# Performance work log

Hardware: AMD Instinct MI355X
Metric: run time of the kernel (lower is better)

The kernel has to match this reference:

```python
import jax, jax.numpy as jnp
import numpy as np

DIM = 512
HEADS = 8
HEAD_DIM = DIM // HEADS
WINDOW = 128
TOKEN_SELF_ATTN_VALUE = -5e4  # lucidrains local-attention constant for shared_qk self mask


def setup_inputs() -> dict:
    key = jax.random.key(0)
    k1, k2, k3, k4 = jax.random.split(key, 4)
    B, N = 4, 8192
    x = jax.random.normal(k1, (B, N, DIM), dtype=jnp.float32)
    w_qkv = jax.random.normal(k2, (3 * DIM, DIM), dtype=jnp.float32) * (DIM ** -0.5)
    w_proj = jax.random.normal(k3, (DIM, DIM), dtype=jnp.float32) * (DIM ** -0.5)
    b_proj = jax.random.normal(k4, (DIM,), dtype=jnp.float32) * 0.01
    return {"x": x, "w_qkv": w_qkv, "w_proj": w_proj, "b_proj": b_proj}


def _look_around(b):
    # b: [B,H,nw,w,D] -> [B,H,nw,2w,D] = concat(prev_window, cur_window); window 0 padded with zeros
    padded = jnp.pad(b, ((0, 0), (0, 0), (1, 0), (0, 0), (0, 0)))
    return jnp.concatenate([padded[:, :, :-1], b], axis=3)


def _local_attn(q, k, v):
    # causal sliding-window attention, window=128, look_backward=1, shared_qk
    B, H, N, D = q.shape
    w = WINDOW
    nw = N // w
    scale = D ** -0.5
    # shared_qk: l2-normalize keys (F.normalize, eps=1e-12)
    k = k / jnp.clip(jnp.linalg.norm(k, axis=-1, keepdims=True), 1e-12, None)

    bq = q.reshape(B, H, nw, w, D)
    bk = _look_around(k.reshape(B, H, nw, w, D))  # [B,H,nw,2w,D]
    bv = _look_around(v.reshape(B, H, nw, w, D))

    t = jnp.arange(N).reshape(nw, w)
    t_pad = jnp.pad(t, ((1, 0), (0, 0)), constant_values=-1)
    bq_t = t                                         # [nw, w]
    bq_k = jnp.concatenate([t_pad[:-1], t], axis=1)  # [nw, 2w]

    sim = jnp.einsum('bhwie,bhwje->bhwij', bq, bk) * scale  # [B,H,nw,w,2w]

    self_mask = bq_t[:, :, None] == bq_k[:, None, :]
    causal_mask = bq_t[:, :, None] < bq_k[:, None, :]
    pad_mask = (bq_k == -1)[:, None, :]
    mask_value = -jnp.finfo(sim.dtype).max
    sim = jnp.where(self_mask, TOKEN_SELF_ATTN_VALUE, sim)
    sim = jnp.where(causal_mask | pad_mask, mask_value, sim)

    attn = jax.nn.softmax(sim, axis=-1)  # dropout is identity in eval mode
    out = jnp.einsum('bhwij,bhwje->bhwie', attn, bv)
    return out.reshape(B, H, N, D)


def reference(x, w_qkv, w_proj, b_proj):
    B, N, C = x.shape
    qkv = x @ w_qkv.T  # [B,N,3C]
    q, k, v = jnp.split(qkv, 3, axis=-1)
    to_heads = lambda t: t.reshape(B, N, HEADS, HEAD_DIM).transpose(0, 2, 1, 3)
    out = _local_attn(to_heads(q), to_heads(k), to_heads(v))  # [B,H,N,D]
    out = out.transpose(0, 2, 1, 3).reshape(B, N, C)
    return out @ w_proj.T + b_proj
```

## Files before the change

### kernel.cpp

```cpp
#include <hip/hip_runtime.h>
#include <stdint.h>

typedef uint16_t u16;
typedef __bf16 bf16x8 __attribute__((ext_vector_type(8)));
typedef float f32x4 __attribute__((ext_vector_type(4)));
typedef uint16_t u16x4 __attribute__((ext_vector_type(4)));
typedef uint16_t u16x8 __attribute__((ext_vector_type(8)));

typedef __attribute__((address_space(1))) void as1_void;
typedef __attribute__((address_space(3))) void as3_void;

__device__ __forceinline__ float bf2f(u16 b) {
    union { uint32_t u; float f; } v; v.u = ((uint32_t)b) << 16; return v.f;
}
__device__ __forceinline__ u16 f2bf(float f) {
    union { float f; uint32_t u; } v; v.f = f;
    uint32_t u = v.u;
    u += 0x7fffu + ((u >> 16) & 1u);
    return (u16)(u >> 16);
}
__device__ __forceinline__ void gload_lds16(const u16* g, u16* l) {
    __builtin_amdgcn_global_load_lds((as1_void*)g, (as3_void*)l, 16, 0, 0);
}

__global__ __launch_bounds__(256) void cvt_w(
    const float* __restrict__ wq, u16* __restrict__ wqb,
    const float* __restrict__ wp, u16* __restrict__ wpb)
{
    const float* src; u16* dst; int base;
    const int b = blockIdx.x;
    if (b < 384) { src = wq; dst = wqb; base = b; }
    else         { src = wp; dst = wpb; base = b - 384; }
    const size_t i = ((size_t)base * 256 + threadIdx.x) * 8;
    f32x4 a = *(const f32x4*)(src + i);
    f32x4 c = *(const f32x4*)(src + i + 4);
    u16x8 o;
    o[0] = f2bf(a[0]); o[1] = f2bf(a[1]); o[2] = f2bf(a[2]); o[3] = f2bf(a[3]);
    o[4] = f2bf(c[0]); o[5] = f2bf(c[1]); o[6] = f2bf(c[2]); o[7] = f2bf(c[3]);
    *(u16x8*)(dst + i) = o;
}

template<int NT, bool NORMK>
__global__ __launch_bounds__(256, 3) void gemm_a32(
    const float* __restrict__ A, int lda,
    const u16* __restrict__ B, int ldb,
    u16* __restrict__ C, int ldc)
{
    __shared__ float lA[2][128 * 32];
    __shared__ u16   lB[2][128 * 32];

    const int tid  = threadIdx.x;
    const int lane = tid & 63;
    const int wave = tid >> 6;
    const int wr = (wave >> 1) * 64;
    const int wc = (wave & 1) * 64;
    const int cl = lane & 15;
    const int gr = lane >> 4;

    int fid = blockIdx.y * gridDim.x + blockIdx.x;
    const int nwg = gridDim.x * gridDim.y;
    fid = (fid & 7) * (nwg >> 3) + (fid >> 3);
    const int row0 = (fid / gridDim.x) * 128;
    const int col0 = (fid % gridDim.x) * 128;

    const int srowA = lane >> 3;
    const int schA  = ((lane & 7) - srowA) & 7;
    const int srowB = lane >> 2;
    const int schB  = ((lane & 3) - ((lane >> 3) & 3)) & 3;

    f32x4 acc[4][4] = {};

    auto STAGE = [&](int t, int d) {
        const int k0 = t * 32;
        #pragma unroll
        for (int i = 0; i < 4; ++i) {
            const int Rg = wave * 32 + i * 8;
            gload_lds16((const u16*)(A + (size_t)(row0 + Rg + srowA) * lda + k0 + schA * 4),
                        (u16*)&lA[d][Rg * 32]);
        }
        #pragma unroll
        for (int i = 0; i < 2; ++i) {
            const int Rg = wave * 16 + i * 64;
            gload_lds16(B + (size_t)(col0 + Rg + srowB) * ldb + k0 + schB * 8,
                        &lB[d][Rg * 32]);
        }
    };

    STAGE(0, 0);
    STAGE(1, 1);
    #pragma unroll
    for (int t = 0; t < NT; ++t) {
        if (t < NT - 1) asm volatile("s_waitcnt vmcnt(6)" ::: "memory");
        else            asm volatile("s_waitcnt vmcnt(0)" ::: "memory");
        __builtin_amdgcn_s_barrier();
        const float* la = lA[t & 1];
        const u16*   lb = lB[t & 1];

        bf16x8 af[4], bfv[4];
        #pragma unroll
        for (int m = 0; m < 4; ++m) {
            const int ra = wr + m * 16 + cl;
            const int s0 = (gr * 2 + ra) & 7;
            const int s1 = (gr * 2 + 1 + ra) & 7;
            const f32x4 x0 = *(const f32x4*)&la[ra * 32 + s0 * 4];
            const f32x4 x1 = *(const f32x4*)&la[ra * 32 + s1 * 4];
            bf16x8 t8;
            t8[0] = (__bf16)x0[0]; t8[1] = (__bf16)x0[1];
            t8[2] = (__bf16)x0[2]; t8[3] = (__bf16)x0[3];
            t8[4] = (__bf16)x1[0]; t8[5] = (__bf16)x1[1];
            t8[6] = (__bf16)x1[2]; t8[7] = (__bf16)x1[3];
            af[m] = t8;
        }
        #pragma unroll
        for (int n = 0; n < 4; ++n) {
            const int rb = wc + n * 16 + cl;
            bfv[n] = *(const bf16x8*)&lb[rb * 32 + ((gr + (rb >> 1)) & 3) * 8];
        }
        __builtin_amdgcn_s_setprio(1);
        #pragma unroll
        for (int m = 0; m < 4; ++m)
            #pragma unroll
            for (int n = 0; n < 4; ++n)
                acc[m][n] = __builtin_amdgcn_mfma_f32_16x16x32_bf16(af[m], bfv[n], acc[m][n], 0, 0, 0);
        __builtin_amdgcn_s_setprio(0);
        __builtin_amdgcn_s_barrier();
        if (t + 2 < NT) STAGE(t + 2, t & 1);
    }

    if constexpr (NORMK) {
        if (col0 + wc >= 512 && col0 + wc < 1024) {
            #pragma unroll
            for (int m = 0; m < 4; ++m)
                #pragma unroll
                for (int j = 0; j < 4; ++j) {
                    float ss = 0.f;
                    #pragma unroll
                    for (int n = 0; n < 4; ++n) ss += acc[m][n][j] * acc[m][n][j];
                    ss += __shfl_xor(ss, 1);
                    ss += __shfl_xor(ss, 2);
                    ss += __shfl_xor(ss, 4);
                    ss += __shfl_xor(ss, 8);
                    const float scl = 1.f / fmaxf(sqrtf(ss), 1e-12f);
                    #pragma unroll
                    for (int n = 0; n < 4; ++n) acc[m][n][j] *= scl;
                }
        }
    }

    #pragma unroll
    for (int m = 0; m < 4; ++m) {
        const int r = row0 + wr + m * 16 + gr * 4;
        #pragma unroll
        for (int n = 0; n < 4; ++n) {
            const int c = col0 + wc + n * 16 + cl;
            #pragma unroll
            for (int j = 0; j < 4; ++j)
                C[(size_t)(r + j) * ldc + c] = f2bf(acc[m][n][j]);
        }
    }
}

template<int NT, bool C_F32, bool NORMK>
__global__ __launch_bounds__(512) void gemm256(
    const u16* __restrict__ A, int lda,
    const u16* __restrict__ B, int ldb,
    const float* __restrict__ bias,
    void* __restrict__ Cv, int ldc)
{
    __shared__ u16 lA[2][256 * 64];
    __shared__ u16 lB[2][256 * 64];

    const int tid  = threadIdx.x;
    const int lane = tid & 63;
    const int wave = tid >> 6;
    const int wm = wave >> 2;
    const int wn = wave & 3;
    const int cl = lane & 15;
    const int gr = lane >> 4;

    int fid = blockIdx.y * gridDim.x + blockIdx.x;
    const int nwg = gridDim.x * gridDim.y;
    fid = (fid & 7) * (nwg >> 3) + (fid >> 3);
    const int row0 = (fid / gridDim.x) * 256;
    const int col0 = (fid % gridDim.x) * 256;

    const int srow   = lane >> 3;
    const int schunk = ((lane & 7) - srow) & 7;

    f32x4 acc[8][4] = {};

    auto STAGE = [&](int t, int d) {
        const int k0 = t * 64;
        #pragma unroll
        for (int i = 0; i < 4; ++i) {
            const int Rg = wave * 32 + i * 8;
            gload_lds16(A + (size_t)(row0 + Rg + srow) * lda + k0 + schunk * 8,
                        &lA[d][Rg * 64]);
            gload_lds16(B + (size_t)(col0 + Rg + srow) * ldb + k0 + schunk * 8,
                        &lB[d][Rg * 64]);
        }
    };

    auto COMPUTE = [&](int d) {
        const u16* la = lA[d];
        const u16* lb = lB[d];
        bf16x8 bfrag[2][4];
        #pragma unroll
        for (int kk = 0; kk < 2; ++kk)
            #pragma unroll
            for (int n = 0; n < 4; ++n) {
                const int rb = wn * 64 + n * 16 + cl;
                bfrag[kk][n] = *(const bf16x8*)(lb + rb * 64 + (((kk * 4 + gr + rb) & 7) * 8));
            }
        __builtin_amdgcn_s_setprio(1);
        #pragma unroll
        for (int m = 0; m < 8; ++m) {
            const int ra = wm * 128 + m * 16 + cl;
            const bf16x8 a0 = *(const bf16x8*)(la + ra * 64 + (((gr + ra) & 7) * 8));
            const bf16x8 a1 = *(const bf16x8*)(la + ra * 64 + (((4 + gr + ra) & 7) * 8));
            #pragma unroll
            for (int n = 0; n < 4; ++n)
                acc[m][n] = __builtin_amdgcn_mfma_f32_16x16x32_bf16(a0, bfrag[0][n], acc[m][n], 0, 0, 0);
            #pragma unroll
            for (int n = 0; n < 4; ++n)
                acc[m][n] = __builtin_amdgcn_mfma_f32_16x16x32_bf16(a1, bfrag[1][n], acc[m][n], 0, 0, 0);
        }
        __builtin_amdgcn_s_setprio(0);
    };

    STAGE(0, 0);
    STAGE(1, 1);
    #pragma unroll
    for (int t = 0; t < NT; ++t) {
        if (t < NT - 1) asm volatile("s_waitcnt vmcnt(8)" ::: "memory");
        else            asm volatile("s_waitcnt vmcnt(0)" ::: "memory");
        __builtin_amdgcn_s_barrier();
        COMPUTE(t & 1);
        __builtin_amdgcn_s_barrier();
        if (t + 2 < NT) STAGE(t + 2, t & 1);
    }

    if constexpr (NORMK) {
        if (col0 + wn * 64 >= 512 && col0 + wn * 64 < 1024) {
            #pragma unroll
            for (int m = 0; m < 8; ++m)
                #pragma unroll
                for (int j = 0; j < 4; ++j) {
                    float ss = 0.f;
                    #pragma unroll
                    for (int n = 0; n < 4; ++n) ss += acc[m][n][j] * acc[m][n][j];
                    ss += __shfl_xor(ss, 1);
                    ss += __shfl_xor(ss, 2);
                    ss += __shfl_xor(ss, 4);
                    ss += __shfl_xor(ss, 8);
                    const float scl = 1.f / fmaxf(sqrtf(ss), 1e-12f);
                    #pragma unroll
                    for (int n = 0; n < 4; ++n) acc[m][n][j] *= scl;
                }
        }
    }

    #pragma unroll
    for (int m = 0; m < 8; ++m) {
        const int r = row0 + wm * 128 + m * 16 + gr * 4;
        #pragma unroll
        for (int n = 0; n < 4; ++n) {
            const int c = col0 + wn * 64 + n * 16 + cl;
            const float bv = bias ? bias[c] : 0.f;
            #pragma unroll
            for (int j = 0; j < 4; ++j) {
                const float val = acc[m][n][j] + bv;
                if constexpr (C_F32) ((float*)Cv)[(size_t)(r + j) * ldc + c] = val;
                else                 ((u16*)Cv)[(size_t)(r + j) * ldc + c] = f2bf(val);
            }
        }
    }
}

template<bool A_F32, bool C_F32, bool NORMK>
__global__ __launch_bounds__(256) void gemm_bt_f32(
    const void* __restrict__ Av, int lda,
    const float* __restrict__ B, int ldb,
    const float* __restrict__ bias,
    void* __restrict__ Cv, int ldc,
    int K)
{
    __shared__ u16 lA[128 * 32];
    __shared__ u16 lB[128 * 32];

    const int tid  = threadIdx.x;
    const int lane = tid & 63;
    const int wave = tid >> 6;
    const int wr   = (wave >> 1) * 64;
    const int wc   = (wave & 1) * 64;
    const int row0 = blockIdx.y * 128;
    const int col0 = blockIdx.x * 128;

    f32x4 acc[4][4] = {};

    for (int k0 = 0; k0 < K; k0 += 32) {
        #pragma unroll
        for (int i = 0; i < 4; ++i) {
            const int idx = i * 256 + tid;
            const int r = idx >> 3;
            const int p = (idx & 7) * 4;
            u16x4 a4, b4;
            if constexpr (A_F32) {
                const float* Af = (const float*)Av;
                f32x4 va = *(const f32x4*)(Af + (size_t)(row0 + r) * lda + k0 + p);
                a4[0] = f2bf(va[0]); a4[1] = f2bf(va[1]); a4[2] = f2bf(va[2]); a4[3] = f2bf(va[3]);
            } else {
                const u16* Ab = (const u16*)Av;
                a4 = *(const u16x4*)(Ab + (size_t)(row0 + r) * lda + k0 + p);
            }
            {
                f32x4 vb = *(const f32x4*)(B + (size_t)(col0 + r) * ldb + k0 + p);
                b4[0] = f2bf(vb[0]); b4[1] = f2bf(vb[1]); b4[2] = f2bf(vb[2]); b4[3] = f2bf(vb[3]);
            }
            *(u16x4*)&lA[r * 32 + p] = a4;
            *(u16x4*)&lB[r * 32 + p] = b4;
        }
        __syncthreads();

        bf16x8 af[4], bfv[4];
        #pragma unroll
        for (int m = 0; m < 4; ++m)
            af[m] = *(const bf16x8*)(lA + (wr + m * 16 + (lane & 15)) * 32 + (lane >> 4) * 8);
        #pragma unroll
        for (int n = 0; n < 4; ++n)
            bfv[n] = *(const bf16x8*)(lB + (wc + n * 16 + (lane & 15)) * 32 + (lane >> 4) * 8);
        #pragma unroll
        for (int m = 0; m < 4; ++m)
            #pragma unroll
            for (int n = 0; n < 4; ++n)
                acc[m][n] = __builtin_amdgcn_mfma_f32_16x16x32_bf16(af[m], bfv[n], acc[m][n], 0, 0, 0);
        __syncthreads();
    }

    if constexpr (NORMK) {
        if (col0 >= 512 && col0 < 1024) {
            #pragma unroll
            for (int m = 0; m < 4; ++m)
                #pragma unroll
                for (int j = 0; j < 4; ++j) {
                    float ss = 0.f;
                    #pragma unroll
                    for (int n = 0; n < 4; ++n) ss += acc[m][n][j] * acc[m][n][j];
                    ss += __shfl_xor(ss, 1);
                    ss += __shfl_xor(ss, 2);
                    ss += __shfl_xor(ss, 4);
                    ss += __shfl_xor(ss, 8);
                    const float scl = 1.f / fmaxf(sqrtf(ss), 1e-12f);
                    #pragma unroll
                    for (int n = 0; n < 4; ++n) acc[m][n][j] *= scl;
                }
        }
    }

    #pragma unroll
    for (int m = 0; m < 4; ++m) {
        const int r = row0 + wr + m * 16 + ((lane >> 4) << 2);
        #pragma unroll
        for (int n = 0; n < 4; ++n) {
            const int c = col0 + wc + n * 16 + (lane & 15);
            const float bv = bias ? bias[c] : 0.f;
            #pragma unroll
            for (int j = 0; j < 4; ++j) {
                const float val = acc[m][n][j] + bv;
                if constexpr (C_F32) ((float*)Cv)[(size_t)(r + j) * ldc + c] = val;
                else                 ((u16*)Cv)[(size_t)(r + j) * ldc + c] = f2bf(val);
            }
        }
    }
}

__global__ __launch_bounds__(512, 4) void attn_kernel(const u16* qkv, u16* o)
{
    constexpr int CC = 1536;
    constexpr int NTOK = 8192;
    constexpr int KP = 72;
    constexpr int VP = 136;
    constexpr int PP = 136;
    __shared__ u16 kn[128 * KP];
    __shared__ u16 vT[64 * VP];
    __shared__ u16 Pl[128 * PP];

    const int tid  = threadIdx.x;
    const int lane = tid & 63;
    const int wave = tid >> 6;
    const int cl = lane & 15;
    const int gr = lane >> 4;

    int blk = blockIdx.x;
    blk = (blk & 7) * (gridDim.x >> 3) + (blk >> 3);

    const int iw  = blk & 63;
    const int h   = (blk >> 6) & 7;
    const int b   = blk >> 9;

    const int tq0 = iw * 128;
    const size_t rowbase = (size_t)b * NTOK;
    const u16* qbase = qkv + rowbase * CC + h * 64;
    const u16* kbase = qbase + 512;
    const u16* vbase = qbase + 1024;

    const int wrow = wave * 16;
    bf16x8 qf[2];
    #pragma unroll
    for (int kk = 0; kk < 2; ++kk)
        qf[kk] = *(const bf16x8*)(qbase + (size_t)(tq0 + wrow + cl) * CC + kk * 32 + gr * 8);

    f32x4 oacc[4] = {};
    float m_run[4] = {-3.0e38f, -3.0e38f, -3.0e38f, -3.0e38f};
    float l_run[4] = {0.f, 0.f, 0.f, 0.f};

    for (int c = 0; c < 2; ++c) {
        const int tkc = tq0 - 128 + c * 128;

        #pragma unroll
        for (int p = 0; p < 2; ++p) {
            const int id = tid + p * 512;
            const int row = id >> 3, dc = id & 7;
            u16x8 v8 = {};
            if (tkc >= 0) v8 = *(const u16x8*)(kbase + (size_t)(tkc + row) * CC + dc * 8);
            *(u16x8*)&kn[row * KP + dc * 8] = v8;
        }
        #pragma unroll
        for (int p = 0; p < 2; ++p) {
            const int id = tid + p * 512;
            const int key = id & 127, dc = id >> 7;
            u16x8 v8 = {};
            if (tkc >= 0) v8 = *(const u16x8*)(vbase + (size_t)(tkc + key) * CC + dc * 8);
            #pragma unroll
            for (int e = 0; e < 8; ++e) vT[(dc * 8 + e) * VP + key] = v8[e];
        }
        __syncthreads();

        f32x4 s[8] = {};
        #pragma unroll
        for (int n = 0; n < 8; ++n)
            #pragma unroll
            for (int kk = 0; kk < 2; ++kk) {
                const bf16x8 kf = *(const bf16x8*)&kn[(n * 16 + cl) * KP + kk * 32 + gr * 8];
                s[n] = __builtin_amdgcn_mfma_f32_16x16x32_bf16(qf[kk], kf, s[n], 0, 0, 0);
            }

        float pmax[4] = {-3.0e38f, -3.0e38f, -3.0e38f, -3.0e38f};
        #pragma unroll
        for (int n = 0; n < 8; ++n) {
            const int tkk = tkc + n * 16 + cl;
            const bool pad = tkk < 0;
            #pragma unroll
            for (int j = 0; j < 4; ++j) {
                const int tq = tq0 + wrow + gr * 4 + j;
                float sv = s[n][j] * 0.125f;
                const int rel = tkk - tq;
                sv = (rel == 0) ? -5.0e4f : sv;
                sv = (rel > 0 || pad) ? -6.0e4f : sv;
                s[n][j] = sv;
                pmax[j] = fmaxf(pmax[j], sv);
            }
        }
        float cold[4];
        #pragma unroll
        for (int j = 0; j < 4; ++j) {
            pmax[j] = fmaxf(pmax[j], __shfl_xor(pmax[j], 1));
            pmax[j] = fmaxf(pmax[j], __shfl_xor(pmax[j], 2));
            pmax[j] = fmaxf(pmax[j], __shfl_xor(pmax[j], 4));
            pmax[j] = fmaxf(pmax[j], __shfl_xor(pmax[j], 8));
            const float mn = fmaxf(m_run[j], pmax[j]);
            cold[j] = __expf(m_run[j] - mn);
            m_run[j] = mn;
            l_run[j] *= cold[j];
        }
        #pragma unroll
        for (int n = 0; n < 8; ++n)
            #pragma unroll
            for (int j = 0; j < 4; ++j) {
                const float p = __expf(s[n][j] - m_run[j]);
                s[n][j] = p;
                l_run[j] += p;
            }
        #pragma unroll
        for (int n = 0; n < 4; ++n) {
            f32x4 t = oacc[n];
            t[0] *= cold[0]; t[1] *= cold[1]; t[2] *= cold[2]; t[3] *= cold[3];
            oacc[n] = t;
        }
        #pragma unroll
        for (int n = 0; n < 8; ++n)
            #pragma unroll
            for (int j = 0; j < 4; ++j)
                Pl[(wrow + gr * 4 + j) * PP + n * 16 + cl] = f2bf(s[n][j]);
        __syncthreads();

        #pragma unroll
        for (int kk = 0; kk < 4; ++kk) {
            const bf16x8 pa = *(const bf16x8*)&Pl[(wrow + cl) * PP + kk * 32 + gr * 8];
            #pragma unroll
            for (int n = 0; n < 4; ++n) {
                const bf16x8 vb = *(const bf16x8*)&vT[(n * 16 + cl) * VP + kk * 32 + gr * 8];
                oacc[n] = __builtin_amdgcn_mfma_f32_16x16x32_bf16(pa, vb, oacc[n], 0, 0, 0);
            }
        }
        __syncthreads();
    }

    float inv[4];
    #pragma unroll
    for (int j = 0; j < 4; ++j) {
        l_run[j] += __shfl_xor(l_run[j], 1);
        l_run[j] += __shfl_xor(l_run[j], 2);
        l_run[j] += __shfl_xor(l_run[j], 4);
        l_run[j] += __shfl_xor(l_run[j], 8);
        inv[j] = 1.f / l_run[j];
    }
    u16* obase = o + rowbase * CC + h * 64;
    const int r0 = tq0 + wrow + gr * 4;
    #pragma unroll
    for (int n = 0; n < 4; ++n) {
        const int d = n * 16 + cl;
        #pragma unroll
        for (int j = 0; j < 4; ++j)
            obase[(size_t)(r0 + j) * CC + d] = f2bf(oacc[n][j] * inv[j]);
    }
}

extern "C" void kernel_launch(void* const* d_in, const int* in_sizes, int n_in,
                              void* d_out, int out_size, void* d_ws, size_t ws_size,
                              hipStream_t stream)
{
    (void)in_sizes; (void)n_in; (void)out_size;
    const float* x      = (const float*)d_in[0];
    const float* w_qkv  = (const float*)d_in[1];
    const float* w_proj = (const float*)d_in[2];
    const float* b_proj = (const float*)d_in[3];
    float* out = (float*)d_out;

    const int BN = 4 * 8192;
    const size_t qkv_b = (size_t)BN * 1536 * 2;
    const size_t wq_b  = (size_t)1536 * 512 * 2;
    const size_t wp_b  = (size_t)512 * 512 * 2;

    uint8_t* p = (uint8_t*)d_ws;
    u16* qkv = (u16*)p;

    if (ws_size >= qkv_b + wq_b + wp_b) {
        u16* wqb = (u16*)(p + qkv_b);
        u16* wpb = (u16*)(p + qkv_b + wq_b);
        cvt_w<<<512, 256, 0, stream>>>(w_qkv, wqb, w_proj, wpb);
        gemm_a32<16, true><<<dim3(12, 256), 256, 0, stream>>>(
            x, 512, wqb, 512, qkv, 1536);
        attn_kernel<<<dim3(4 * 8 * 64), 512, 0, stream>>>(qkv, qkv);
        gemm256<8, true, false><<<dim3(2, 128), 512, 0, stream>>>(
            qkv, 1536, wpb, 512, b_proj, out, 512);
    } else {
        gemm_bt_f32<true, false, true><<<dim3(12, BN / 128), 256, 0, stream>>>(
            x, 512, w_qkv, 512, nullptr, qkv, 1536, 512);
        attn_kernel<<<dim3(4 * 8 * 64), 512, 0, stream>>>(qkv, qkv);
        gemm_bt_f32<false, true, false><<<dim3(4, BN / 128), 256, 0, stream>>>(
            qkv, 1536, w_proj, 512, b_proj, out, 512, 512);
    }
}
```

Before: 180.5 us.

## Stage fp32 A tile through registers and store as bf16 in LDS

```diff
diff --git a/kernel.cpp b/kernel.cpp
--- a/kernel.cpp
+++ b/kernel.cpp
@@ -41,13 +41,13 @@
 }
 
 template<int NT, bool NORMK>
-__global__ __launch_bounds__(256, 3) void gemm_a32(
+__global__ __launch_bounds__(256, 4) void gemm_rs(
     const float* __restrict__ A, int lda,
     const u16* __restrict__ B, int ldb,
     u16* __restrict__ C, int ldc)
 {
-    __shared__ float lA[2][128 * 32];
-    __shared__ u16   lB[2][128 * 32];
+    __shared__ u16 lA[2][128 * 32];
+    __shared__ u16 lB[2][128 * 32];
 
     const int tid  = threadIdx.x;
     const int lane = tid & 63;
@@ -63,54 +63,57 @@
     const int row0 = (fid / gridDim.x) * 128;
     const int col0 = (fid % gridDim.x) * 128;
 
-    const int srowA = lane >> 3;
-    const int schA  = ((lane & 7) - srowA) & 7;
+    const int arow = tid >> 1;
+    const int ah   = tid & 1;
     const int srowB = lane >> 2;
     const int schB  = ((lane & 3) - ((lane >> 3) & 3)) & 3;
 
+    f32x4 S[4];
+
     f32x4 acc[4][4] = {};
 
-    auto STAGE = [&](int t, int d) {
-        const int k0 = t * 32;
-        #pragma unroll
-        for (int i = 0; i < 4; ++i) {
-            const int Rg = wave * 32 + i * 8;
-            gload_lds16((const u16*)(A + (size_t)(row0 + Rg + srowA) * lda + k0 + schA * 4),
-                        (u16*)&lA[d][Rg * 32]);
-        }
+    auto A_LOAD = [&](int t) {
+        const float* g = A + (size_t)(row0 + arow) * lda + t * 32 + ah * 16;
+        S[0] = *(const f32x4*)(g);
+        S[1] = *(const f32x4*)(g + 4);
+        S[2] = *(const f32x4*)(g + 8);
+        S[3] = *(const f32x4*)(g + 12);
+    };
+    auto A_STORE = [&](int d) {
+        u16x8 w0, w1;
+        w0[0] = f2bf(S[0][0]); w0[1] = f2bf(S[0][1]); w0[2] = f2bf(S[0][2]); w0[3] = f2bf(S[0][3]);
+        w0[4] = f2bf(S[1][0]); w0[5] = f2bf(S[1][1]); w0[6] = f2bf(S[1][2]); w0[7] = f2bf(S[1][3]);
+        w1[0] = f2bf(S[2][0]); w1[1] = f2bf(S[2][1]); w1[2] = f2bf(S[2][2]); w1[3] = f2bf(S[2][3]);
+        w1[4] = f2bf(S[3][0]); w1[5] = f2bf(S[3][1]); w1[6] = f2bf(S[3][2]); w1[7] = f2bf(S[3][3]);
+        *(u16x8*)&lA[d][arow * 32 + ah * 16]     = w0;
+        *(u16x8*)&lA[d][arow * 32 + ah * 16 + 8] = w1;
+    };
+    auto B_STAGE = [&](int t, int d) {
         #pragma unroll
         for (int i = 0; i < 2; ++i) {
             const int Rg = wave * 16 + i * 64;
-            gload_lds16(B + (size_t)(col0 + Rg + srowB) * ldb + k0 + schB * 8,
+            gload_lds16(B + (size_t)(col0 + Rg + srowB) * ldb + t * 32 + schB * 8,
                         &lB[d][Rg * 32]);
         }
     };
 
-    STAGE(0, 0);
-    STAGE(1, 1);
+    A_LOAD(0); A_STORE(0); B_STAGE(0, 0);
+    A_LOAD(1); A_STORE(1); B_STAGE(1, 1);
+
     #pragma unroll
     for (int t = 0; t < NT; ++t) {
-        if (t < NT - 1) asm volatile("s_waitcnt vmcnt(6)" ::: "memory");
-        else            asm volatile("s_waitcnt vmcnt(0)" ::: "memory");
+        if (t < NT - 1) asm volatile("s_waitcnt vmcnt(2) lgkmcnt(0)" ::: "memory");
+        else            asm volatile("s_waitcnt vmcnt(0) lgkmcnt(0)" ::: "memory");
         __builtin_amdgcn_s_barrier();
-        const float* la = lA[t & 1];
-        const u16*   lb = lB[t & 1];
-
+
+        if (t + 2 < NT) { A_LOAD(t + 2); asm volatile("" ::: "memory"); }
+
+        const u16* la = lA[t & 1];
+        const u16* lb = lB[t & 1];
         bf16x8 af[4], bfv[4];
         #pragma unroll
-        for (int m = 0; m < 4; ++m) {
-            const int ra = wr + m * 16 + cl;
-            const int s0 = (gr * 2 + ra) & 7;
-            const int s1 = (gr * 2 + 1 + ra) & 7;
-            const f32x4 x0 = *(const f32x4*)&la[ra * 32 + s0 * 4];
-            const f32x4 x1 = *(const f32x4*)&la[ra * 32 + s1 * 4];
-            bf16x8 t8;
-            t8[0] = (__bf16)x0[0]; t8[1] = (__bf16)x0[1];
-            t8[2] = (__bf16)x0[2]; t8[3] = (__bf16)x0[3];
-            t8[4] = (__bf16)x1[0]; t8[5] = (__bf16)x1[1];
-            t8[6] = (__bf16)x1[2]; t8[7] = (__bf16)x1[3];
-            af[m] = t8;
-        }
+        for (int m = 0; m < 4; ++m)
+            af[m] = *(const bf16x8*)&la[(wr + m * 16 + cl) * 32 + gr * 8];
         #pragma unroll
         for (int n = 0; n < 4; ++n) {
             const int rb = wc + n * 16 + cl;
@@ -124,7 +127,8 @@
                 acc[m][n] = __builtin_amdgcn_mfma_f32_16x16x32_bf16(af[m], bfv[n], acc[m][n], 0, 0, 0);
         __builtin_amdgcn_s_setprio(0);
         __builtin_amdgcn_s_barrier();
-        if (t + 2 < NT) STAGE(t + 2, t & 1);
+
+        if (t + 2 < NT) { A_STORE(t & 1); B_STAGE(t + 2, t & 1); }
     }
 
     if constexpr (NORMK) {
@@ -549,7 +553,7 @@
         u16* wqb = (u16*)(p + qkv_b);
         u16* wpb = (u16*)(p + qkv_b + wq_b);
         cvt_w<<<512, 256, 0, stream>>>(w_qkv, wqb, w_proj, wpb);
-        gemm_a32<16, true><<<dim3(12, 256), 256, 0, stream>>>(
+        gemm_rs<16, true><<<dim3(12, 256), 256, 0, stream>>>(
             x, 512, wqb, 512, qkv, 1536);
         attn_kernel<<<dim3(4 * 8 * 64), 512, 0, stream>>>(qkv, qkv);
         gemm256<8, true, false><<<dim3(2, 128), 512, 0, stream>>>(
```

After: 208.2 us. 15.3% more time.
